# Kernel optimization log

Hardware: AMD Instinct MI355X
Metric: run time of the kernel (lower is better)

The kernel has to match this reference:

```python
import jax, jax.numpy as jnp
import numpy as np

B, S, HID = 2, 2048, 1024
H, KV, D = 16, 8, 64
NDIM = 2          # position_ids.shape[-1]
EPS = 1e-6
SCALING = 1.0


def _rms_norm(x, w=None, eps=EPS):
    # matches _RMSNorm: fp32 compute, optional learnable scale
    xf = x.astype(jnp.float32)
    n = xf * jax.lax.rsqrt(jnp.mean(xf * xf, axis=-1, keepdims=True) + eps)
    if w is not None:
        n = n * w.astype(jnp.float32)
    return n.astype(x.dtype)


def _rotate_half(x):
    d = x.shape[-1] // 2
    return jnp.concatenate([-x[..., d:], x[..., :d]], axis=-1)


def _apply_multidim_rope(x, cos, sin, ndim):
    # x: [B,S,h,D]; cos/sin: [B,S,D]; unsqueeze_dim=2 broadcasts over heads
    num_channels = x.shape[-1]
    cpd = 2 * (num_channels // (2 * ndim))  # channels per RoPE dimension
    outs = []
    for k in range(ndim):
        sl = slice(k * cpd, (k + 1) * cpd)
        xk = x[..., sl]
        ck = cos[..., sl][:, :, None, :]
        sk = sin[..., sl][:, :, None, :]
        outs.append(xk * ck + _rotate_half(xk) * sk)
    return jnp.concatenate(outs, axis=-1)


def setup_inputs() -> dict:
    key = jax.random.key(0)
    ks = jax.random.split(key, 10)
    scale = 0.02
    return {
        "hidden_states": jax.random.normal(ks[0], (B, S, HID), jnp.float32),
        "cos": jax.random.normal(ks[1], (B, S, D), jnp.float32),
        "sin": jax.random.normal(ks[2], (B, S, D), jnp.float32),
        "position_ids": jax.random.randint(ks[3], (B, S, NDIM), 0, 64, jnp.int64),
        "Wq": jax.random.normal(ks[4], (HID, H * D), jnp.float32) * scale,
        "Wk": jax.random.normal(ks[5], (HID, KV * D), jnp.float32) * scale,
        "Wv": jax.random.normal(ks[6], (HID, KV * D), jnp.float32) * scale,
        "Wo": jax.random.normal(ks[7], (H * D, HID), jnp.float32) * scale,
        "q_norm_w": jnp.ones((D,), jnp.float32),
        "k_norm_w": jnp.ones((D,), jnp.float32),
    }


def reference(hidden_states, cos, sin, position_ids, Wq, Wk, Wv, Wo, q_norm_w, k_norm_w):
    ndim = position_ids.shape[-1]
    bsz, seq_len, _ = hidden_states.shape

    q = (hidden_states @ Wq).reshape(bsz, seq_len, H, D)
    q = _rms_norm(q, q_norm_w)
    q = _apply_multidim_rope(q, cos, sin, ndim)
    q = jnp.transpose(q, (0, 2, 1, 3))  # [B,H,S,D]

    k = (hidden_states @ Wk).reshape(bsz, seq_len, KV, D)
    k = _rms_norm(k, k_norm_w)
    k = _apply_multidim_rope(k, cos, sin, ndim)
    k = jnp.transpose(k, (0, 2, 1, 3))  # [B,KV,S,D]

    v = (hidden_states @ Wv).reshape(bsz, seq_len, KV, D)
    v = _rms_norm(v, None)  # v_norm has no scale
    v = jnp.transpose(v, (0, 2, 1, 3))  # [B,KV,S,D]

    groups = H // KV
    if groups > 1:
        k = jnp.repeat(k, groups, axis=1)  # [B,H,S,D]
        v = jnp.repeat(v, groups, axis=1)

    scores = jnp.einsum("bhqd,bhkd->bhqk", q, k) * SCALING
    attn = jax.nn.softmax(scores.astype(jnp.float32), axis=-1).astype(q.dtype)
    out = jnp.einsum("bhqk,bhkd->bhqd", attn, v)
    out = jnp.transpose(out, (0, 2, 1, 3)).reshape(bsz, seq_len, H * D)
    return out @ Wo
```

## Files before the change

### kernel.cpp

```cpp
#include <hip/hip_runtime.h>

#define PB 2
#define PS 2048
#define PHID 1024
#define PH 16
#define PKV 8
#define PD 64
#define PM (PB*PS)
#define PR (PB*PH*PS)

typedef _Float16 f16_t;
typedef _Float16 f16x8 __attribute__((ext_vector_type(8)));
typedef _Float16 f16x2 __attribute__((ext_vector_type(2)));
typedef __fp16 fp16v2 __attribute__((ext_vector_type(2)));
typedef float f32x4 __attribute__((ext_vector_type(4)));

#define MFMAH(a,b,c)  __builtin_amdgcn_mfma_f32_16x16x32_f16((a),(b),(c),0,0,0)
#define LOG2E 1.44269504f

__device__ __forceinline__ void gl16(const f16_t* g, f16_t* l) {
  __builtin_amdgcn_global_load_lds(
      (const __attribute__((address_space(1))) void*)g,
      (__attribute__((address_space(3))) void*)l, 16, 0, 0);
}

__global__ __launch_bounds__(256)
void convert_hs(const float* __restrict__ hs, f16_t* __restrict__ hf)
{
  const size_t i = ((size_t)blockIdx.x * 256 + threadIdx.x) * 8;
  float4 a = *(const float4*)&hs[i];
  float4 b = *(const float4*)&hs[i + 4];
  float xs[8] = {a.x, a.y, a.z, a.w, b.x, b.y, b.z, b.w};
  f16x8 v;
  #pragma unroll
  for (int j = 0; j < 8; ++j) v[j] = (f16_t)xs[j];
  *(f16x8*)&hf[i] = v;
}

__global__ __launch_bounds__(256)
void convert_w(const float* __restrict__ Wq, const float* __restrict__ Wk,
               const float* __restrict__ Wv, const float* __restrict__ Wo,
               f16_t* __restrict__ wtT)
{
  __shared__ float Tt[64][68];
  const int tid = threadIdx.x;
  const int slot = blockIdx.x >> 4, k0 = (blockIdx.x & 15) * 64;

  const float* src; int N, ncol0, orow0;
  if (slot < 16)      { src = Wq; N = 1024; ncol0 = slot*64;      orow0 = slot*64; }
  else if (slot < 24) { src = Wk; N = 512;  ncol0 = (slot-16)*64; orow0 = 1024 + (slot-16)*64; }
  else if (slot < 32) { src = Wv; N = 512;  ncol0 = (slot-24)*64; orow0 = 1536 + (slot-24)*64; }
  else                { src = Wo; N = 1024; ncol0 = (slot-32)*64; orow0 = 2048 + (slot-32)*64; }

  const int tk = tid >> 6, tn = tid & 63;
  #pragma unroll
  for (int i = 0; i < 16; ++i)
    Tt[tn][tk*16 + i] = src[(size_t)(k0 + tk*16 + i) * N + ncol0 + tn];
  __syncthreads();

  const int n = tid >> 2, kc = (tid & 3) * 16;
  f16x8 a0, a1;
  #pragma unroll
  for (int i = 0; i < 8; ++i) {
    a0[i] = (f16_t)Tt[n][kc + i];
    a1[i] = (f16_t)Tt[n][kc + 8 + i];
  }
  const size_t ob = (size_t)(orow0 + n) * 1024 + k0 + kc;
  *(f16x8*)&wtT[ob]     = a0;
  *(f16x8*)&wtT[ob + 8] = a1;
}

__global__ __launch_bounds__(256)
void qkv_kernel(const f16_t* __restrict__ hsf, const f16_t* __restrict__ wtT,
                const float* __restrict__ cosp, const float* __restrict__ sinp,
                const float* __restrict__ qnw, const float* __restrict__ knw,
                f16_t* __restrict__ q_o, f16_t* __restrict__ k_o,
                f16_t* __restrict__ vt_o)
{
  __shared__ __align__(16) f16_t Ah[128][64];
  __shared__ __align__(16) f16_t Bh[128][64];

  const int tid = threadIdx.x;
  const int lane = tid & 63, wave = tid >> 6;
  const int lo16 = lane & 15, hi4 = lane >> 4;
  const int lin = blockIdx.x;
  const int swz = (lin & 7) * 64 + (lin >> 3);
  const int m0 = (swz >> 4) * 128;
  const int ws = swz & 15;
  const int orow = ws * 128;

  int kind, hd0;
  if (ws < 8)       { kind = 0; hd0 = ws*2; }
  else if (ws < 12) { kind = 1; hd0 = (ws-8)*2; }
  else              { kind = 2; hd0 = (ws-12)*2; }

  f32x4 acc[2][8];
  #pragma unroll
  for (int qb = 0; qb < 2; ++qb)
    #pragma unroll
    for (int j = 0; j < 8; ++j) acc[qb][j] = f32x4{0.f, 0.f, 0.f, 0.f};

  const int ri = lane >> 3, pc = lane & 7;
  const int lcs = (pc ^ ri) * 8;
  size_t aoff4[4]; f16_t* aldst4[4];
  size_t boff4[4]; f16_t* bldst4[4];
  #pragma unroll
  for (int q = 0; q < 4; ++q) {
    aoff4[q] = (size_t)(m0 + wave*32 + q*8 + ri) * PHID + lcs;
    aldst4[q] = &Ah[wave*32 + q*8][0];
    boff4[q] = (size_t)(orow + wave*32 + q*8 + ri) * 1024 + lcs;
    bldst4[q] = &Bh[wave*32 + q*8][0];
  }

  const int rsw = lo16 & 7;

  for (int k0 = 0; k0 < PHID; k0 += 64) {
    __syncthreads();
    #pragma unroll
    for (int q = 0; q < 4; ++q) gl16(hsf + aoff4[q] + k0, aldst4[q]);
    #pragma unroll
    for (int q = 0; q < 4; ++q) gl16(wtT + boff4[q] + k0, bldst4[q]);
    __syncthreads();

    #pragma unroll
    for (int t = 0; t < 2; ++t) {
      const int ccol = ((t*4 + hi4) ^ rsw) * 8;
      f16x8 ah[2];
      #pragma unroll
      for (int qb = 0; qb < 2; ++qb)
        ah[qb] = *(const f16x8*)&Ah[wave*32 + qb*16 + lo16][ccol];
      #pragma unroll
      for (int j = 0; j < 8; ++j) {
        f16x8 bh = *(const f16x8*)&Bh[j*16 + lo16][ccol];
        #pragma unroll
        for (int qb = 0; qb < 2; ++qb)
          acc[qb][j] = MFMAH(ah[qb], bh, acc[qb][j]);
      }
    }
  }

  float nwv[4];
  #pragma unroll
  for (int jj = 0; jj < 4; ++jj)
    nwv[jj] = (kind == 0) ? qnw[lo16 + 16*jj]
            : (kind == 1) ? knw[lo16 + 16*jj] : 1.0f;

  #pragma unroll
  for (int qb = 0; qb < 2; ++qb) {
    float sc[2][4];
    #pragma unroll
    for (int r = 0; r < 4; ++r) {
      float s0 = 0.f, s1 = 0.f;
      #pragma unroll
      for (int j = 0; j < 4; ++j) {
        s0 += acc[qb][j][r]   * acc[qb][j][r];
        s1 += acc[qb][j+4][r] * acc[qb][j+4][r];
      }
      #pragma unroll
      for (int m = 1; m < 16; m <<= 1) {
        s0 += __shfl_xor(s0, m);
        s1 += __shfl_xor(s1, m);
      }
      sc[0][r] = 1.0f / sqrtf(s0 * (1.0f/64.0f) + 1e-6f);
      sc[1][r] = 1.0f / sqrtf(s1 * (1.0f/64.0f) + 1e-6f);
    }

    float y[8][4];
    #pragma unroll
    for (int j = 0; j < 8; ++j)
      #pragma unroll
      for (int r = 0; r < 4; ++r)
        y[j][r] = acc[qb][j][r] * sc[j>>2][r] * nwv[j&3];

    if (kind == 2) {
      #pragma unroll
      for (int r = 0; r < 4; ++r) {
        int mg = m0 + wave*32 + qb*16 + hi4*4 + r;
        int b = mg >> 11, sq = mg & 2047;
        int g = sq & 63;
        int sp = (g & 3) | (((g >> 4) & 1) << 2) | (((g >> 2) & 1) << 3)
               | (((g >> 3) & 1) << 4) | (g & 32);
        int sq2 = (sq & ~63) | sp;
        #pragma unroll
        for (int j = 0; j < 8; ++j) {
          int d = lo16 + 16*(j & 3), hd = hd0 + (j >> 2);
          vt_o[((size_t)((b*PKV + hd)*PD + d))*PS + sq2] = (f16_t)y[j][r];
        }
      }
    } else {
      #pragma unroll
      for (int r = 0; r < 4; ++r) {
        int mg = m0 + wave*32 + qb*16 + hi4*4 + r;
        int b = mg >> 11, sq = mg & 2047;
        const float* cp = &cosp[(size_t)mg * PD];
        const float* sp = &sinp[(size_t)mg * PD];
        float z[8];
        #pragma unroll
        for (int j = 0; j < 8; ++j) {
          int d = lo16 + 16*(j & 3);
          float c = cp[d], s = sp[d];
          float rot = (j & 1) ? y[j-1][r] : -y[j+1][r];
          z[j] = y[j][r] * c + rot * s;
        }
        #pragma unroll
        for (int j = 0; j < 8; ++j) {
          int d = lo16 + 16*(j & 3), hd = hd0 + (j >> 2);
          if (kind == 0) {
            size_t idx = ((size_t)(b*PH + hd)*PS + sq)*PD + d;
            q_o[idx] = (f16_t)(z[j] * LOG2E);
          } else {
            size_t idx = ((size_t)(b*PKV + hd)*PS + sq)*PD + d;
            k_o[idx] = (f16_t)z[j];
          }
        }
      }
    }
  }
}

__global__ __launch_bounds__(256, 3)
void attn_kernel(const f16_t* __restrict__ q_g, const f16_t* __restrict__ k_g,
                 const f16_t* __restrict__ vt_g,
                 f16_t* __restrict__ op, float2* __restrict__ ml)
{
  __shared__ __align__(16) char lds_raw[32768];
  f16_t (*Ks)[64][64] = (f16_t (*)[64][64])lds_raw;
  f16_t (*Vs)[64][64] = (f16_t (*)[64][64])(lds_raw + 16384);
  f16_t (*Ob)[72]     = (f16_t (*)[72])lds_raw;

  const int tid = threadIdx.x, lane = tid & 63, wave = tid >> 6;
  const int lo16 = lane & 15, hi4 = lane >> 4;
  const int lin = blockIdx.x;
  const int swz = (lin & 7) * 128 + (lin >> 3);
  const int qt = swz & 15;
  const int bh = (swz >> 4) & 31;
  const int ks = swz >> 9;
  const int b = bh >> 4, h = bh & 15, kvh = h >> 1;

  f16x8 qf[2][2];
  #pragma unroll
  for (int qb = 0; qb < 2; ++qb) {
    const size_t qbase = ((size_t)(b*PH + h)*PS + qt*128 + wave*32 + qb*16 + lo16) * PD;
    #pragma unroll
    for (int t = 0; t < 2; ++t)
      qf[qb][t] = *(const f16x8*)&q_g[qbase + t*32 + hi4*8];
  }

  f32x4 o[2][4], lsum[2];
  float mq[2] = {0.f, 0.f};
  #pragma unroll
  for (int qb = 0; qb < 2; ++qb) {
    lsum[qb] = f32x4{0.f, 0.f, 0.f, 0.f};
    #pragma unroll
    for (int j = 0; j < 4; ++j) o[qb][j] = f32x4{0.f, 0.f, 0.f, 0.f};
  }

  f16x8 ONES;
  #pragma unroll
  for (int e = 0; e < 8; ++e) ONES[e] = (f16_t)1.0f;

  const int ri = lane >> 3;
  const int lcs = ((lane & 7) ^ ri) * 8;
  const size_t kbase = (size_t)(b*PKV + kvh) * PS * PD + (size_t)ks * 1024 * PD;
  const size_t vbase = (size_t)(b*PKV + kvh) * PD * PS + (size_t)ks * 1024;

  auto STAGE = [&](int kt, int buf) {
    const f16_t* kp = k_g + kbase + (size_t)kt * 64 * PD;
    const f16_t* vp = vt_g + vbase + kt * 64;
    #pragma unroll
    for (int i = 0; i < 2; ++i) {
      const int st = wave*2 + i;
      gl16(kp + (st*8 + ri)*PD + lcs, &Ks[buf][st*8][0]);
      gl16(vp + (size_t)(st*8 + ri)*PS + lcs, &Vs[buf][st*8][0]);
    }
  };

  STAGE(0, 0);
  int cur = 0;
  const int rsw = lo16 & 7;

  for (int kt = 0; kt < 16; ++kt) {
    __syncthreads();
    if (kt + 1 < 16) STAGE(kt + 1, cur ^ 1);

    f32x4 sacc[2][4];
    __builtin_amdgcn_s_setprio(1);
    #pragma unroll
    for (int j = 0; j < 4; ++j) {
      f16x8 kf0 = *(const f16x8*)&Ks[cur][j*16 + lo16][(hi4 ^ rsw) * 8];
      f16x8 kf1 = *(const f16x8*)&Ks[cur][j*16 + lo16][((4 + hi4) ^ rsw) * 8];
      #pragma unroll
      for (int qb = 0; qb < 2; ++qb) {
        f32x4 mc = {-mq[qb], -mq[qb], -mq[qb], -mq[qb]};
        sacc[qb][j] = MFMAH(kf1, qf[qb][1], MFMAH(kf0, qf[qb][0], mc));
      }
    }
    __builtin_amdgcn_s_setprio(0);

    f16x8 pa[2][2];
    #pragma unroll
    for (int qb = 0; qb < 2; ++qb) {
      float m0_ = fmaxf(fmaxf(sacc[qb][0][0], sacc[qb][0][1]), sacc[qb][0][2]);
      float m1_ = fmaxf(fmaxf(sacc[qb][0][3], sacc[qb][1][0]), sacc[qb][1][1]);
      float m2_ = fmaxf(fmaxf(sacc[qb][1][2], sacc[qb][1][3]), sacc[qb][2][0]);
      float m3_ = fmaxf(fmaxf(sacc[qb][2][1], sacc[qb][2][2]), sacc[qb][2][3]);
      float m4_ = fmaxf(fmaxf(sacc[qb][3][0], sacc[qb][3][1]), sacc[qb][3][2]);
      float tm  = fmaxf(fmaxf(m0_, m1_), m2_);
      tm = fmaxf(fmaxf(tm, m3_), m4_);
      tm = fmaxf(tm, sacc[qb][3][3]);
      tm = fmaxf(tm, __shfl_xor(tm, 16));
      tm = fmaxf(tm, __shfl_xor(tm, 32));

      if (!__all(tm <= 8.0f)) {
        float tmx = fmaxf(tm, 0.f);
        float alpha = __builtin_amdgcn_exp2f(-tmx);
        lsum[qb] *= alpha;
        #pragma unroll
        for (int jd = 0; jd < 4; ++jd) o[qb][jd] *= alpha;
        mq[qb] += tmx;
        #pragma unroll
        for (int t = 0; t < 2; ++t) {
          union { fp16v2 h[4]; f16x8 v; } u;
          #pragma unroll
          for (int pr = 0; pr < 2; ++pr) {
            float p0 = __builtin_amdgcn_exp2f(sacc[qb][2*t+pr][0] - tmx);
            float p1 = __builtin_amdgcn_exp2f(sacc[qb][2*t+pr][1] - tmx);
            float p2 = __builtin_amdgcn_exp2f(sacc[qb][2*t+pr][2] - tmx);
            float p3 = __builtin_amdgcn_exp2f(sacc[qb][2*t+pr][3] - tmx);
            u.h[pr*2]   = __builtin_amdgcn_cvt_pkrtz(p0, p1);
            u.h[pr*2+1] = __builtin_amdgcn_cvt_pkrtz(p2, p3);
          }
          pa[qb][t] = u.v;
        }
      } else {
        #pragma unroll
        for (int t = 0; t < 2; ++t) {
          union { fp16v2 h[4]; f16x8 v; } u;
          #pragma unroll
          for (int pr = 0; pr < 2; ++pr) {
            float p0 = __builtin_amdgcn_exp2f(sacc[qb][2*t+pr][0]);
            float p1 = __builtin_amdgcn_exp2f(sacc[qb][2*t+pr][1]);
            float p2 = __builtin_amdgcn_exp2f(sacc[qb][2*t+pr][2]);
            float p3 = __builtin_amdgcn_exp2f(sacc[qb][2*t+pr][3]);
            u.h[pr*2]   = __builtin_amdgcn_cvt_pkrtz(p0, p1);
            u.h[pr*2+1] = __builtin_amdgcn_cvt_pkrtz(p2, p3);
          }
          pa[qb][t] = u.v;
        }
      }
    }

    __builtin_amdgcn_s_setprio(1);
    #pragma unroll
    for (int jd = 0; jd < 4; ++jd) {
      #pragma unroll
      for (int t = 0; t < 2; ++t) {
        f16x8 vf = *(const f16x8*)&Vs[cur][jd*16 + lo16][((t*4 + hi4) ^ rsw) * 8];
        #pragma unroll
        for (int qb = 0; qb < 2; ++qb)
          o[qb][jd] = MFMAH(vf, pa[qb][t], o[qb][jd]);
      }
    }
    #pragma unroll
    for (int qb = 0; qb < 2; ++qb)
      #pragma unroll
      for (int t = 0; t < 2; ++t)
        lsum[qb] = MFMAH(ONES, pa[qb][t], lsum[qb]);
    __builtin_amdgcn_s_setprio(0);

    cur ^= 1;
  }

  __syncthreads();
  const int rbase = bh*PS + qt*128 + wave*32;
  if (hi4 == 0) {
    #pragma unroll
    for (int qb = 0; qb < 2; ++qb)
      ml[(size_t)ks*PR + rbase + qb*16 + lo16] = float2{mq[qb], lsum[qb][0]};
  }
  #pragma unroll
  for (int qb = 0; qb < 2; ++qb) {
    float inv = 1.0f / lsum[qb][0];
    #pragma unroll
    for (int jd = 0; jd < 4; ++jd)
      #pragma unroll
      for (int rp = 0; rp < 2; ++rp)
        *(f16x2*)&Ob[wave*32 + qb*16 + lo16][jd*16 + hi4*4 + 2*rp] =
            f16x2{(f16_t)(o[qb][jd][2*rp] * inv), (f16_t)(o[qb][jd][2*rp+1] * inv)};
  }
  {
    const int row = lane >> 1, half = lane & 1;
    const size_t gb_ = ((size_t)ks*PR + rbase + row) * PD + half*32;
    #pragma unroll
    for (int c = 0; c < 4; ++c)
      *(f16x8*)&op[gb_ + c*8] = *(const f16x8*)&Ob[wave*32 + row][half*32 + c*8];
  }
}

__global__ __launch_bounds__(256)
void merge_kernel(const f16_t* __restrict__ op, const float2* __restrict__ ml,
                  f16_t* __restrict__ ao)
{
  const int gid = blockIdx.x * 256 + threadIdx.x;
  const int row = gid >> 3, oct = gid & 7;
  float2 e0 = ml[row], e1 = ml[PR + row];
  float M = fmaxf(e0.x, e1.x);
  float c0 = __builtin_amdgcn_exp2f(e0.x - M) * e0.y;
  float c1 = __builtin_amdgcn_exp2f(e1.x - M) * e1.y;
  float inv = 1.0f / (c0 + c1);
  c0 *= inv; c1 *= inv;
  f16x8 a = *(const f16x8*)&op[(size_t)row*PD + oct*8];
  f16x8 bq = *(const f16x8*)&op[(size_t)(PR + row)*PD + oct*8];
  f16x8 r;
  #pragma unroll
  for (int i = 0; i < 8; ++i)
    r[i] = (f16_t)(c0 * (float)a[i] + c1 * (float)bq[i]);
  const int bh = row >> 11, sq = row & 2047;
  const int b = bh >> 4, h = bh & 15;
  *(f16x8*)&ao[((size_t)(b*PS + sq))*PHID + h*PD + oct*8] = r;
}

__global__ __launch_bounds__(256)
void oproj_kernel(const f16_t* __restrict__ ao, const f16_t* __restrict__ woT,
                  float* __restrict__ out)
{
  __shared__ __align__(16) f16_t As[128][40], Bs[64][40];
  const int tid = threadIdx.x;
  const int lane = tid & 63, wave = tid >> 6;
  const int lo16 = lane & 15, hi4 = lane >> 4;
  const int lin = blockIdx.x;
  const int swz = (lin & 7) * 64 + (lin >> 3);
  const int m0 = (swz >> 4) * 128;
  const int col0 = (swz & 15) * 64;

  f32x4 acc[2][4];
  #pragma unroll
  for (int qb = 0; qb < 2; ++qb)
    #pragma unroll
    for (int j = 0; j < 4; ++j) acc[qb][j] = f32x4{0.f, 0.f, 0.f, 0.f};

  const int ar = tid >> 1, akc = (tid & 1) * 16;
  const int bn = tid & 63, bkc = (tid >> 6) * 8;

  f16x8 gA0, gA1, gB;
  auto LOADA = [&](int k0) {
    const f16_t* ap = &ao[(size_t)(m0 + ar) * PHID + k0 + akc];
    gA0 = *(const f16x8*)ap;
    gA1 = *(const f16x8*)(ap + 8);
  };
  auto LOADB = [&](int k0) {
    gB = *(const f16x8*)&woT[(size_t)(col0 + bn) * 1024 + k0 + bkc];
  };
  LOADA(0); LOADB(0);

  for (int k0 = 0; k0 < PHID; k0 += 32) {
    __syncthreads();
    *(f16x8*)&As[ar][akc]     = gA0;
    *(f16x8*)&As[ar][akc + 8] = gA1;
    *(f16x8*)&Bs[bn][bkc]     = gB;
    if (k0 + 32 < PHID) { LOADA(k0 + 32); LOADB(k0 + 32); }
    __syncthreads();
    {
      f16x8 a[2];
      #pragma unroll
      for (int qb = 0; qb < 2; ++qb)
        a[qb] = *(const f16x8*)&As[wave*32 + qb*16 + lo16][hi4*8];
      #pragma unroll
      for (int j = 0; j < 4; ++j) {
        f16x8 bb = *(const f16x8*)&Bs[j*16 + lo16][hi4*8];
        #pragma unroll
        for (int qb = 0; qb < 2; ++qb)
          acc[qb][j] = MFMAH(a[qb], bb, acc[qb][j]);
      }
    }
  }

  #pragma unroll
  for (int qb = 0; qb < 2; ++qb)
    #pragma unroll
    for (int r = 0; r < 4; ++r) {
      int mg = m0 + wave*32 + qb*16 + hi4*4 + r;
      #pragma unroll
      for (int j = 0; j < 4; ++j)
        out[(size_t)mg*PHID + col0 + lo16 + 16*j] = acc[qb][j][r];
    }
}

extern "C" void kernel_launch(void* const* d_in, const int* in_sizes, int n_in,
                              void* d_out, int out_size, void* d_ws, size_t ws_size,
                              hipStream_t stream) {
  (void)in_sizes; (void)n_in; (void)out_size; (void)ws_size;
  const float* hs   = (const float*)d_in[0];
  const float* cosp = (const float*)d_in[1];
  const float* sinp = (const float*)d_in[2];
  const float* Wq   = (const float*)d_in[4];
  const float* Wk   = (const float*)d_in[5];
  const float* Wv   = (const float*)d_in[6];
  const float* Wo   = (const float*)d_in[7];
  const float* qnw  = (const float*)d_in[8];
  const float* knw  = (const float*)d_in[9];
  float* out = (float*)d_out;

  const size_t QN = (size_t)PB*PH*PS*PD;
  const size_t KN = (size_t)PB*PKV*PS*PD;
  const size_t HN = (size_t)PM*PHID;
  char* wsb = (char*)d_ws;
  f16_t*  qv  = (f16_t*)wsb;
  f16_t*  kv  = qv + QN;
  f16_t*  vt  = kv + KN;
  f16_t*  hsf = vt + KN;
  f16_t*  wtT = hsf + HN;
  f16_t*  op  = wtT + (size_t)3072*1024;
  float2* ml  = (float2*)(op + 2*QN);
  f16_t*  ao  = qv;
  const f16_t* woT = wtT + (size_t)2048*1024;

  convert_hs<<<dim3(2048), 256, 0, stream>>>(hs, hsf);
  convert_w <<<dim3(768),  256, 0, stream>>>(Wq, Wk, Wv, Wo, wtT);
  qkv_kernel<<<dim3(512),  256, 0, stream>>>(hsf, wtT, cosp, sinp,
                                             qnw, knw, qv, kv, vt);
  attn_kernel<<<dim3(1024), 256, 0, stream>>>(qv, kv, vt, op, ml);
  merge_kernel<<<dim3(PR*8/256), 256, 0, stream>>>(op, ml, ao);
  oproj_kernel<<<dim3(512), 256, 0, stream>>>(ao, woT, out);
}
```

Measured before the change: 118.7 us.

## Use direct global-to-LDS loads with XOR swizzle in output projection; raise attn occupancy

The output projection GEMM now stages A and B tiles into LDS with global_load_lds instead of register round-trips, doubles the K step to 64, and applies an XOR column swizzle to avoid bank conflicts. It drops the register prefetch, so loads are no longer overlapped with compute and each step waits on the LDS fill. The attention kernel's launch bounds also change from 3 to 4 blocks per CU, which may force register spills.

```diff
diff --git a/kernel.cpp b/kernel.cpp
--- a/kernel.cpp
+++ b/kernel.cpp
@@ -218,7 +218,7 @@
   }
 }
 
-__global__ __launch_bounds__(256, 3)
+__global__ __launch_bounds__(256, 4)
 void attn_kernel(const f16_t* __restrict__ q_g, const f16_t* __restrict__ k_g,
                  const f16_t* __restrict__ vt_g,
                  f16_t* __restrict__ op, float2* __restrict__ ml)
@@ -424,7 +424,9 @@
 void oproj_kernel(const f16_t* __restrict__ ao, const f16_t* __restrict__ woT,
                   float* __restrict__ out)
 {
-  __shared__ __align__(16) f16_t As[128][40], Bs[64][40];
+  __shared__ __align__(16) f16_t As[128][64];
+  __shared__ __align__(16) f16_t Bs[64][64];
+
   const int tid = threadIdx.x;
   const int lane = tid & 63, wave = tid >> 6;
   const int lo16 = lane & 15, hi4 = lane >> 4;
@@ -439,35 +441,41 @@
     #pragma unroll
     for (int j = 0; j < 4; ++j) acc[qb][j] = f32x4{0.f, 0.f, 0.f, 0.f};
 
-  const int ar = tid >> 1, akc = (tid & 1) * 16;
-  const int bn = tid & 63, bkc = (tid >> 6) * 8;
-
-  f16x8 gA0, gA1, gB;
-  auto LOADA = [&](int k0) {
-    const f16_t* ap = &ao[(size_t)(m0 + ar) * PHID + k0 + akc];
-    gA0 = *(const f16x8*)ap;
-    gA1 = *(const f16x8*)(ap + 8);
-  };
-  auto LOADB = [&](int k0) {
-    gB = *(const f16x8*)&woT[(size_t)(col0 + bn) * 1024 + k0 + bkc];
-  };
-  LOADA(0); LOADB(0);
-
-  for (int k0 = 0; k0 < PHID; k0 += 32) {
+  const int ri = lane >> 3, pc = lane & 7;
+  const int lcs = (pc ^ ri) * 8;
+  size_t aoff4[4]; f16_t* aldst4[4];
+  #pragma unroll
+  for (int q = 0; q < 4; ++q) {
+    aoff4[q] = (size_t)(m0 + wave*32 + q*8 + ri) * PHID + lcs;
+    aldst4[q] = &As[wave*32 + q*8][0];
+  }
+  size_t boff[2]; int brow[2];
+  #pragma unroll
+  for (int q = 0; q < 2; ++q) {
+    brow[q] = wave*16 + q*8;
+    boff[q] = (size_t)(col0 + brow[q] + ri) * 1024 + lcs;
+  }
+
+  const int rsw = lo16 & 7;
+
+  for (int k0 = 0; k0 < PHID; k0 += 64) {
     __syncthreads();
-    *(f16x8*)&As[ar][akc]     = gA0;
-    *(f16x8*)&As[ar][akc + 8] = gA1;
-    *(f16x8*)&Bs[bn][bkc]     = gB;
-    if (k0 + 32 < PHID) { LOADA(k0 + 32); LOADB(k0 + 32); }
+    #pragma unroll
+    for (int q = 0; q < 4; ++q) gl16(ao + aoff4[q] + k0, aldst4[q]);
+    #pragma unroll
+    for (int q = 0; q < 2; ++q) gl16(woT + boff[q] + k0, &Bs[brow[q]][0]);
     __syncthreads();
-    {
+
+    #pragma unroll
+    for (int t = 0; t < 2; ++t) {
+      const int ccol = ((t*4 + hi4) ^ rsw) * 8;
       f16x8 a[2];
       #pragma unroll
       for (int qb = 0; qb < 2; ++qb)
-        a[qb] = *(const f16x8*)&As[wave*32 + qb*16 + lo16][hi4*8];
+        a[qb] = *(const f16x8*)&As[wave*32 + qb*16 + lo16][ccol];
       #pragma unroll
       for (int j = 0; j < 4; ++j) {
-        f16x8 bb = *(const f16x8*)&Bs[j*16 + lo16][hi4*8];
+        f16x8 bb = *(const f16x8*)&Bs[j*16 + lo16][ccol];
         #pragma unroll
         for (int qb = 0; qb < 2; ++qb)
           acc[qb][j] = MFMAH(a[qb], bb, acc[qb][j]);
```

Result: slower. 138.2 us (+16.5%).
